# Performance work log

Hardware: AMD Instinct MI355X
Metric: run time of the kernel (lower is better)

## Reference

```python
import jax, jax.numpy as jnp
from jax import lax
import numpy as np


def _lstm_layer(x, Wih, Whh, bih, bhh):
    """Single-direction LSTM layer, PyTorch gate order (i, f, g, o).
    x: [B, T, D_in] -> hidden sequence [B, T, H]."""
    B, T, _ = x.shape
    H = Whh.shape[1]
    # Precompute input contribution for all timesteps: [B, T, 4H]
    xw = jnp.einsum('btd,gd->btg', x, Wih) + bih + bhh

    def step(carry, xt):
        h, c = carry
        gates = xt + h @ Whh.T  # [B, 4H]
        i, f, g, o = jnp.split(gates, 4, axis=-1)
        i = jax.nn.sigmoid(i)
        f = jax.nn.sigmoid(f)
        g = jnp.tanh(g)
        o = jax.nn.sigmoid(o)
        c = f * c + i * g
        h = o * jnp.tanh(c)
        return (h, c), h

    h0 = jnp.zeros((B, H), dtype=x.dtype)
    c0 = jnp.zeros((B, H), dtype=x.dtype)
    _, hs = lax.scan(step, (h0, c0), jnp.swapaxes(xw, 0, 1))  # [T, B, H]
    return jnp.swapaxes(hs, 0, 1)  # [B, T, H]


def setup_inputs() -> dict:
    key = jax.random.key(0)
    ks = jax.random.split(key, 9)
    B, T, D, H = 64, 2048, 256, 128
    s = 1.0 / np.sqrt(H)  # PyTorch uniform(-1/sqrt(H), 1/sqrt(H)) init scale
    u = lambda k, shp: jax.random.uniform(k, shp, jnp.float32, -s, s)
    return {
        'x': jax.random.normal(ks[0], (B, T, D), jnp.float32),
        'Wih0': u(ks[1], (4 * H, D)),
        'Whh0': u(ks[2], (4 * H, H)),
        'bih0': u(ks[3], (4 * H,)),
        'bhh0': u(ks[4], (4 * H,)),
        'Wih1': u(ks[5], (4 * H, H)),
        'Whh1': u(ks[6], (4 * H, H)),
        'bih1': u(ks[7], (4 * H,)),
        'bhh1': u(ks[8], (4 * H,)),
    }


def reference(x, Wih0, Whh0, bih0, bhh0, Wih1, Whh1, bih1, bhh1):
    # 2-layer stacked LSTM; inter-layer dropout (p=0.1) is identity at eval.
    h1 = _lstm_layer(x, Wih0, Whh0, bih0, bhh0)
    h2 = _lstm_layer(h1, Wih1, Whh1, bih1, bhh1)
    return h2
```

## Files before the change

kernel.cpp:

```cpp
#include <hip/hip_runtime.h>
#include <hip/hip_bf16.h>

#define H 128
#define FOURH 512
#define BATCH 64
#define SEQ 2048
#define TC SEQ

typedef _Float16 half8 __attribute__((ext_vector_type(8)));
typedef float f32x4 __attribute__((ext_vector_type(4)));

__global__ void prep_kernel(const float* __restrict__ Wih0,
                            const float* __restrict__ bih0, const float* __restrict__ bhh0,
                            const float* __restrict__ bih1, const float* __restrict__ bhh1,
                            float* __restrict__ Wt0,
                            float* __restrict__ b0, float* __restrict__ b1,
                            int* __restrict__ flags) {
    int id = blockIdx.x * 256 + threadIdx.x;
    const int N0 = 256 * 512;
    if (id < N0) {
        int k = id >> 9, n = id & 511;
        Wt0[id] = Wih0[n * 256 + k];
    } else if (id < N0 + 512) {
        int i = id - N0;
        b0[i] = bih0[i] + bhh0[i];
    } else if (id < N0 + 1024) {
        int i = id - (N0 + 512);
        b1[i] = bih1[i] + bhh1[i];
    } else if (id < N0 + 1024 + 8) {
        flags[id - (N0 + 1024)] = 0;
    }
}

#define BM 128
#define BN 128
#define BK 32

__global__ __launch_bounds__(256) void gemm_bias_kernel(
    const float* __restrict__ A, int lda, int rowsPerBatch, int t0,
    const float* __restrict__ Bt, const float* __restrict__ bias,
    float* __restrict__ G, int K, int tcShift)
{
    __shared__ float As[BK][BM + 4];
    __shared__ float Bs[BK][BN];

    const int tid = threadIdx.x;
    const int m0 = blockIdx.y * BM;
    const int n0 = blockIdx.x * BN;
    const int tm = tid >> 4;
    const int tn = tid & 15;
    const int tcMask = (1 << tcShift) - 1;

    const float* aptr[4];
    int ar[4], aq[4];
#pragma unroll
    for (int l = 0; l < 4; ++l) {
        int fidx = tid + l * 256;
        int r = fidx >> 3, q = fidx & 7;
        ar[l] = r; aq[l] = q;
        int m = m0 + r;
        int bi = m >> tcShift;
        int tl = m & tcMask;
        aptr[l] = A + ((size_t)bi * rowsPerBatch + t0 + tl) * lda + q * 4;
    }
    int bkk[4], bq[4];
#pragma unroll
    for (int l = 0; l < 4; ++l) {
        int fidx = tid + l * 256;
        bkk[l] = fidx >> 5; bq[l] = fidx & 31;
    }

    float acc[2][2][4][4];
#pragma unroll
    for (int ri = 0; ri < 2; ++ri)
#pragma unroll
        for (int ci = 0; ci < 2; ++ci)
#pragma unroll
            for (int i = 0; i < 4; ++i)
#pragma unroll
                for (int j = 0; j < 4; ++j) acc[ri][ci][i][j] = 0.f;

    for (int k0 = 0; k0 < K; k0 += BK) {
        __syncthreads();
#pragma unroll
        for (int l = 0; l < 4; ++l) {
            float4 v = *(const float4*)(aptr[l] + k0);
            As[aq[l] * 4 + 0][ar[l]] = v.x;
            As[aq[l] * 4 + 1][ar[l]] = v.y;
            As[aq[l] * 4 + 2][ar[l]] = v.z;
            As[aq[l] * 4 + 3][ar[l]] = v.w;
        }
#pragma unroll
        for (int l = 0; l < 4; ++l) {
            float4 v = *(const float4*)(Bt + (size_t)(k0 + bkk[l]) * FOURH + n0 + bq[l] * 4);
            *(float4*)&Bs[bkk[l]][bq[l] * 4] = v;
        }
        __syncthreads();
#pragma unroll
        for (int kk = 0; kk < BK; ++kk) {
            float a[8], bb[8];
            *(float4*)&a[0] = *(const float4*)&As[kk][tm * 4];
            *(float4*)&a[4] = *(const float4*)&As[kk][64 + tm * 4];
            *(float4*)&bb[0] = *(const float4*)&Bs[kk][tn * 4];
            *(float4*)&bb[4] = *(const float4*)&Bs[kk][64 + tn * 4];
#pragma unroll
            for (int ri = 0; ri < 2; ++ri)
#pragma unroll
                for (int i = 0; i < 4; ++i)
#pragma unroll
                    for (int ci = 0; ci < 2; ++ci)
#pragma unroll
                        for (int j = 0; j < 4; ++j)
                            acc[ri][ci][i][j] = fmaf(a[ri * 4 + i], bb[ci * 4 + j], acc[ri][ci][i][j]);
        }
    }

    float4 bv0 = *(const float4*)&bias[n0 + tn * 4];
    float4 bv1 = *(const float4*)&bias[n0 + 64 + tn * 4];
#pragma unroll
    for (int ri = 0; ri < 2; ++ri)
#pragma unroll
        for (int i = 0; i < 4; ++i) {
            int m = m0 + ri * 64 + tm * 4 + i;
            float* gp = G + (size_t)m * FOURH + n0;
            float4 o0 = make_float4(acc[ri][0][i][0] + bv0.x, acc[ri][0][i][1] + bv0.y,
                                    acc[ri][0][i][2] + bv0.z, acc[ri][0][i][3] + bv0.w);
            float4 o1 = make_float4(acc[ri][1][i][0] + bv1.x, acc[ri][1][i][1] + bv1.y,
                                    acc[ri][1][i][2] + bv1.z, acc[ri][1][i][3] + bv1.w);
            *(float4*)(gp + tn * 4) = o0;
            *(float4*)(gp + 64 + tn * 4) = o1;
        }
}

__device__ __forceinline__ float sigmoid_f(float x) {
    return __builtin_amdgcn_rcpf(1.f + __expf(-x));
}
__device__ __forceinline__ float tanh_f(float x) {
    return 1.f - 2.f * __builtin_amdgcn_rcpf(__expf(2.f * x) + 1.f);
}

#define LDS_BARRIER()                                                \
    do {                                                             \
        asm volatile("s_waitcnt lgkmcnt(0)" ::: "memory");           \
        __builtin_amdgcn_s_barrier();                                \
        __builtin_amdgcn_sched_barrier(0);                           \
    } while (0)

__global__ __launch_bounds__(512, 2) void lstm_fused_kernel(
    const float* __restrict__ G,
    const float* __restrict__ Whh0,
    const float* __restrict__ Wih1,
    const float* __restrict__ Whh1,
    const float* __restrict__ b1,
    _Float16* __restrict__ h1p,
    float* __restrict__ out,
    int* __restrict__ flags)
{
    const int tid = threadIdx.x;
    const int w  = tid >> 6;
    const int l  = tid & 63;
    const int li = l & 15;
    const int q  = l >> 4;
    const int u  = 16 * w + li;
    const int b0 = q * 2;
    const int ab = ((li >> 2) * 2) + (li & 1);

    __shared__ _Float16 hbuf[2][8][136];
    __shared__ float houtb[8][8][132];

    if (blockIdx.x < 8) {
        const int g = blockIdx.x;

        half8 Bf[4][4];
#pragma unroll
        for (int tl = 0; tl < 4; ++tl)
#pragma unroll
            for (int kf = 0; kf < 4; ++kf) {
                const float* wp = Whh0 + (size_t)(tl * 128 + u) * H + kf * 32 + q * 8;
                float4 v0 = *(const float4*)wp;
                float4 v1 = *(const float4*)(wp + 4);
                half8 b;
                b[0] = (_Float16)v0.x; b[1] = (_Float16)v0.y;
                b[2] = (_Float16)v0.z; b[3] = (_Float16)v0.w;
                b[4] = (_Float16)v1.x; b[5] = (_Float16)v1.y;
                b[6] = (_Float16)v1.z; b[7] = (_Float16)v1.w;
                Bf[tl][kf] = b;
            }

        float c0 = 0.f, c1 = 0.f, h0 = 0.f, h1v = 0.f;
        hbuf[0][b0][u]     = (_Float16)0.f;
        hbuf[0][b0 + 1][u] = (_Float16)0.f;

        const float* gb = G + (size_t)(8 * g) * TC * FOURH;
        const int voff0 = b0 * TC * FOURH + u;
        const int voff1 = (b0 + 1) * TC * FOURH + u;

        float G0[8], G1[8], G2[8], G3[8];
        const float* gld = gb;
#pragma unroll
        for (int tl = 0; tl < 4; ++tl) {
            G0[tl * 2 + 0] = gld[voff0 + tl * H];
            G0[tl * 2 + 1] = gld[voff1 + tl * H];
        }
        gld += FOURH;
#pragma unroll
        for (int tl = 0; tl < 4; ++tl) {
            G1[tl * 2 + 0] = gld[voff0 + tl * H];
            G1[tl * 2 + 1] = gld[voff1 + tl * H];
        }
        gld += FOURH;
#pragma unroll
        for (int tl = 0; tl < 4; ++tl) {
            G2[tl * 2 + 0] = gld[voff0 + tl * H];
            G2[tl * 2 + 1] = gld[voff1 + tl * H];
        }
        gld += FOURH;
#pragma unroll
        for (int tl = 0; tl < 4; ++tl) {
            G3[tl * 2 + 0] = gld[voff0 + tl * H];
            G3[tl * 2 + 1] = gld[voff1 + tl * H];
        }
        gld += FOURH;

        _Float16* php = h1p + (size_t)(8 * g + b0) * H + u;
        __syncthreads();

#define P_STEP(PB, GR)                                                            \
    {                                                                             \
        half8 Afr[4];                                                             \
        _Pragma("unroll")                                                         \
        for (int kf = 0; kf < 4; ++kf)                                            \
            Afr[kf] = *(const half8*)&hbuf[PB][ab][kf * 32 + q * 8];              \
        f32x4 acc[4];                                                             \
        _Pragma("unroll")                                                         \
        for (int tl = 0; tl < 4; ++tl) {                                          \
            acc[tl][0] = GR[tl * 2 + 0]; acc[tl][1] = GR[tl * 2 + 1];             \
            acc[tl][2] = 0.f;            acc[tl][3] = 0.f;                        \
        }                                                                         \
        _Pragma("unroll")                                                         \
        for (int tl = 0; tl < 4; ++tl) {                                          \
            GR[tl * 2 + 0] = gld[voff0 + tl * H];                                 \
            GR[tl * 2 + 1] = gld[voff1 + tl * H];                                 \
        }                                                                         \
        gld += FOURH;                                                             \
        _Pragma("unroll")                                                         \
        for (int kf = 0; kf < 4; ++kf)                                            \
            _Pragma("unroll")                                                     \
            for (int tl = 0; tl < 4; ++tl)                                        \
                acc[tl] = __builtin_amdgcn_mfma_f32_16x16x32_f16(Afr[kf], Bf[tl][kf], acc[tl], 0, 0, 0); \
        {                                                                         \
            float ig = sigmoid_f(acc[0][0]);                                      \
            float fg = sigmoid_f(acc[1][0]);                                      \
            float gg = tanh_f(acc[2][0]);                                         \
            float og = sigmoid_f(acc[3][0]);                                      \
            c0 = fmaf(fg, c0, ig * gg);                                           \
            h0 = og * tanh_f(c0);                                                 \
            float ig1 = sigmoid_f(acc[0][1]);                                     \
            float fg1 = sigmoid_f(acc[1][1]);                                     \
            float gg1 = tanh_f(acc[2][1]);                                        \
            float og1 = sigmoid_f(acc[3][1]);                                     \
            c1 = fmaf(fg1, c1, ig1 * gg1);                                        \
            h1v = og1 * tanh_f(c1);                                               \
        }                                                                         \
        hbuf[PB ^ 1][b0][u]     = (_Float16)h0;                                   \
        hbuf[PB ^ 1][b0 + 1][u] = (_Float16)h1v;                                  \
        php[0]   = (_Float16)h0;                                                  \
        php[128] = (_Float16)h1v;                                                 \
        php += BATCH * H;                                                         \
        LDS_BARRIER();                                                            \
    }

        for (int s4 = 0; s4 < TC; s4 += 4) {
            P_STEP(0, G0)
            P_STEP(1, G1)
            P_STEP(0, G2)
            P_STEP(1, G3)
            if ((s4 & 15) == 12) {
                __threadfence();
                __syncthreads();
                if (tid == 0)
                    __hip_atomic_store(&flags[g], s4 + 4, __ATOMIC_RELEASE,
                                       __HIP_MEMORY_SCOPE_AGENT);
            }
        }
#undef P_STEP
    } else {
        const int g = blockIdx.x - 8;

        half8 Bf[4][8];
#pragma unroll
        for (int tl = 0; tl < 4; ++tl)
#pragma unroll
            for (int kf = 0; kf < 8; ++kf) {
                const float* base = (kf < 4) ? Wih1 : Whh1;
                int kk = (kf & 3) * 32 + q * 8;
                const float* wp = base + (size_t)(tl * 128 + u) * H + kk;
                float4 v0 = *(const float4*)wp;
                float4 v1 = *(const float4*)(wp + 4);
                half8 b;
                b[0] = (_Float16)v0.x; b[1] = (_Float16)v0.y;
                b[2] = (_Float16)v0.z; b[3] = (_Float16)v0.w;
                b[4] = (_Float16)v1.x; b[5] = (_Float16)v1.y;
                b[6] = (_Float16)v1.z; b[7] = (_Float16)v1.w;
                Bf[tl][kf] = b;
            }

        float bv[4];
#pragma unroll
        for (int tl = 0; tl < 4; ++tl) bv[tl] = b1[tl * 128 + u];

        float c0 = 0.f, c1 = 0.f, h0, h1v;
        hbuf[0][b0][u]     = (_Float16)0.f;
        hbuf[0][b0 + 1][u] = (_Float16)0.f;

        const _Float16* h1pG = h1p + (size_t)(8 * g + ab) * H + q * 8;
        float* houtBase = out + (size_t)(8 * g) * SEQ * H;

        if (tid == 0) {
            while (__hip_atomic_load(&flags[g], __ATOMIC_ACQUIRE,
                                     __HIP_MEMORY_SCOPE_AGENT) < 32)
                __builtin_amdgcn_s_sleep(2);
        }
        __syncthreads();

        half8 Af0[4], Af1[4];
#pragma unroll
        for (int kf = 0; kf < 4; ++kf)
            Af0[kf] = *(const half8*)(h1pG + kf * 32);
        {
            const _Float16* hp = h1pG + (size_t)(BATCH * H);
#pragma unroll
            for (int kf = 0; kf < 4; ++kf)
                Af1[kf] = *(const half8*)(hp + kf * 32);
        }

#define C_STEP(S, PB, AfU)                                                        \
    {                                                                             \
        half8 Ah[4];                                                              \
        _Pragma("unroll")                                                         \
        for (int kf = 0; kf < 4; ++kf)                                            \
            Ah[kf] = *(const half8*)&hbuf[PB][ab][kf * 32 + q * 8];               \
        f32x4 acc[4];                                                             \
        _Pragma("unroll")                                                         \
        for (int tl = 0; tl < 4; ++tl) {                                          \
            acc[tl][0] = bv[tl]; acc[tl][1] = bv[tl];                             \
            acc[tl][2] = bv[tl]; acc[tl][3] = bv[tl];                             \
        }                                                                         \
        _Pragma("unroll")                                                         \
        for (int kf = 0; kf < 4; ++kf)                                            \
            _Pragma("unroll")                                                     \
            for (int tl = 0; tl < 4; ++tl)                                        \
                acc[tl] = __builtin_amdgcn_mfma_f32_16x16x32_f16(AfU[kf], Bf[tl][kf], acc[tl], 0, 0, 0); \
        {                                                                         \
            int sn = (S) + 2; if (sn > TC - 1) sn = TC - 1;                       \
            const _Float16* hp = h1pG + (size_t)sn * (BATCH * H);                 \
            _Pragma("unroll")                                                     \
            for (int kf = 0; kf < 4; ++kf)                                        \
                AfU[kf] = *(const half8*)(hp + kf * 32);                          \
        }                                                                         \
        _Pragma("unroll")                                                         \
        for (int kf = 0; kf < 4; ++kf)                                            \
            _Pragma("unroll")                                                     \
            for (int tl = 0; tl < 4; ++tl)                                        \
                acc[tl] = __builtin_amdgcn_mfma_f32_16x16x32_f16(Ah[kf], Bf[tl][kf + 4], acc[tl], 0, 0, 0); \
        {                                                                         \
            float ig = sigmoid_f(acc[0][0]);                                      \
            float fg = sigmoid_f(acc[1][0]);                                      \
            float gg = tanh_f(acc[2][0]);                                         \
            float og = sigmoid_f(acc[3][0]);                                      \
            c0 = fmaf(fg, c0, ig * gg);                                           \
            h0 = og * tanh_f(c0);                                                 \
            float ig1 = sigmoid_f(acc[0][1]);                                     \
            float fg1 = sigmoid_f(acc[1][1]);                                     \
            float gg1 = tanh_f(acc[2][1]);                                        \
            float og1 = sigmoid_f(acc[3][1]);                                     \
            c1 = fmaf(fg1, c1, ig1 * gg1);                                        \
            h1v = og1 * tanh_f(c1);                                               \
        }                                                                         \
        hbuf[PB ^ 1][b0][u]     = (_Float16)h0;                                   \
        hbuf[PB ^ 1][b0 + 1][u] = (_Float16)h1v;                                  \
        houtb[(S) & 7][b0][u]     = h0;                                           \
        houtb[(S) & 7][b0 + 1][u] = h1v;                                          \
        LDS_BARRIER();                                                            \
    }

        for (int s4 = 0; s4 < TC; s4 += 4) {
            if (s4 && (s4 & 15) == 0) {
                if (tid == 0) {
                    int tgt = (s4 + 32 > TC) ? TC : s4 + 32;
                    while (__hip_atomic_load(&flags[g], __ATOMIC_ACQUIRE,
                                             __HIP_MEMORY_SCOPE_AGENT) < tgt)
                        __builtin_amdgcn_s_sleep(2);
                }
                __syncthreads();
            }
            C_STEP(s4 + 0, 0, Af0)
            C_STEP(s4 + 1, 1, Af1)
            C_STEP(s4 + 2, 0, Af0)
            C_STEP(s4 + 3, 1, Af1)
            if ((s4 & 7) == 4) {
                int sbase = s4 - 4;
#pragma unroll
                for (int k = 0; k < 4; ++k) {
                    int idx = k * 512 + tid;
                    int u4 = idx & 31;
                    int si = (idx >> 5) & 7;
                    int bi = idx >> 8;
                    float4 v = *(const float4*)&houtb[si][bi][u4 * 4];
                    float* dst = houtBase + (size_t)bi * SEQ * H
                               + (size_t)(sbase + si) * H + u4 * 4;
                    *(float4*)dst = v;
                }
                LDS_BARRIER();
            }
        }
#undef C_STEP
    }
}

extern "C" void kernel_launch(void* const* d_in, const int* in_sizes, int n_in,
                              void* d_out, int out_size, void* d_ws, size_t ws_size,
                              hipStream_t stream) {
    const float* x    = (const float*)d_in[0];
    const float* Wih0 = (const float*)d_in[1];
    const float* Whh0 = (const float*)d_in[2];
    const float* bih0 = (const float*)d_in[3];
    const float* bhh0 = (const float*)d_in[4];
    const float* Wih1 = (const float*)d_in[5];
    const float* Whh1 = (const float*)d_in[6];
    const float* bih1 = (const float*)d_in[7];
    const float* bhh1 = (const float*)d_in[8];
    float* out = (float*)d_out;

    char* ws = (char*)d_ws;
    size_t off = 0;
    auto carve = [&](size_t bytes) -> char* {
        char* p = ws + off;
        off += (bytes + 255) & ~(size_t)255;
        return p;
    };

    float*     Wt0   = (float*)carve(256 * 512 * 4);
    float*     b0v   = (float*)carve(512 * 4);
    float*     b1v   = (float*)carve(512 * 4);
    _Float16*  h1p   = (_Float16*)carve((size_t)SEQ * BATCH * H * 2);
    int*       flags = (int*)carve(8 * 4);
    float*     gbuf  = (float*)carve((size_t)BATCH * SEQ * FOURH * 4 + 16384);

    prep_kernel<<<517, 256, 0, stream>>>(Wih0, bih0, bhh0, bih1, bhh1, Wt0, b0v, b1v, flags);

    dim3 ggrid(FOURH / BN, (BATCH * SEQ) / BM);
    gemm_bias_kernel<<<ggrid, 256, 0, stream>>>(x, 256, SEQ, 0, Wt0, b0v, gbuf, 256, 11);

    lstm_fused_kernel<<<16, 512, 0, stream>>>(gbuf, Whh0, Wih1, Whh1, b1v,
                                              h1p, out, flags);
}
```

Measured before the change: 2.139 ms.

## Offload layer-1 input projection to dedicated blocks with ring-buffered pipeline

```diff
diff --git a/kernel.cpp b/kernel.cpp
--- a/kernel.cpp
+++ b/kernel.cpp
@@ -6,6 +6,9 @@
 #define BATCH 64
 #define SEQ 2048
 #define TC SEQ
+#define RH 1024
+#define RG 128
+#define CCH 32
 
 typedef _Float16 half8 __attribute__((ext_vector_type(8)));
 typedef float f32x4 __attribute__((ext_vector_type(4)));
@@ -27,7 +30,7 @@
     } else if (id < N0 + 1024) {
         int i = id - (N0 + 512);
         b1[i] = bih1[i] + bhh1[i];
-    } else if (id < N0 + 1024 + 8) {
+    } else if (id < N0 + 1024 + 24) {
         flags[id - (N0 + 1024)] = 0;
     }
 }
@@ -153,6 +156,7 @@
     const float* __restrict__ Whh1,
     const float* __restrict__ b1,
     _Float16* __restrict__ h1p,
+    float* __restrict__ G1r,
     float* __restrict__ out,
     int* __restrict__ flags)
 {
@@ -164,6 +168,10 @@
     const int u  = 16 * w + li;
     const int b0 = q * 2;
     const int ab = ((li >> 2) * 2) + (li & 1);
+
+    int* prodF = flags;
+    int* cF    = flags + 8;
+    int* consF = flags + 16;
 
     __shared__ _Float16 hbuf[2][8][136];
     __shared__ float houtb[8][8][132];
@@ -271,6 +279,18 @@
     }
 
         for (int s4 = 0; s4 < TC; s4 += 4) {
+            if ((s4 & 15) == 0 && s4) {
+                php = h1p + (size_t)(s4 & (RH - 1)) * (BATCH * H)
+                    + (size_t)(8 * g + b0) * H + u;
+                if (s4 >= RH) {
+                    if (tid == 0) {
+                        while (__hip_atomic_load(&cF[g], __ATOMIC_ACQUIRE,
+                                                 __HIP_MEMORY_SCOPE_AGENT) < s4 - (RH - CCH))
+                            __builtin_amdgcn_s_sleep(2);
+                    }
+                    __syncthreads();
+                }
+            }
             P_STEP(0, G0)
             P_STEP(1, G1)
             P_STEP(0, G2)
@@ -279,22 +299,20 @@
                 __threadfence();
                 __syncthreads();
                 if (tid == 0)
-                    __hip_atomic_store(&flags[g], s4 + 4, __ATOMIC_RELEASE,
+                    __hip_atomic_store(&prodF[g], s4 + 4, __ATOMIC_RELEASE,
                                        __HIP_MEMORY_SCOPE_AGENT);
             }
         }
 #undef P_STEP
-    } else {
+    } else if (blockIdx.x < 16) {
         const int g = blockIdx.x - 8;
 
-        half8 Bf[4][8];
+        half8 Bf[4][4];
 #pragma unroll
         for (int tl = 0; tl < 4; ++tl)
 #pragma unroll
-            for (int kf = 0; kf < 8; ++kf) {
-                const float* base = (kf < 4) ? Wih1 : Whh1;
-                int kk = (kf & 3) * 32 + q * 8;
-                const float* wp = base + (size_t)(tl * 128 + u) * H + kk;
+            for (int kf = 0; kf < 4; ++kf) {
+                const float* wp = Whh1 + (size_t)(tl * 128 + u) * H + kf * 32 + q * 8;
                 float4 v0 = *(const float4*)wp;
                 float4 v1 = *(const float4*)(wp + 4);
                 half8 b;
@@ -305,64 +323,59 @@
                 Bf[tl][kf] = b;
             }
 
-        float bv[4];
-#pragma unroll
-        for (int tl = 0; tl < 4; ++tl) bv[tl] = b1[tl * 128 + u];
-
         float c0 = 0.f, c1 = 0.f, h0, h1v;
         hbuf[0][b0][u]     = (_Float16)0.f;
         hbuf[0][b0 + 1][u] = (_Float16)0.f;
 
-        const _Float16* h1pG = h1p + (size_t)(8 * g + ab) * H + q * 8;
+        const int goff0 = (8 * g + b0) * FOURH + u;
+        const int goff1 = goff0 + FOURH;
         float* houtBase = out + (size_t)(8 * g) * SEQ * H;
 
         if (tid == 0) {
-            while (__hip_atomic_load(&flags[g], __ATOMIC_ACQUIRE,
+            while (__hip_atomic_load(&cF[g], __ATOMIC_ACQUIRE,
                                      __HIP_MEMORY_SCOPE_AGENT) < 32)
                 __builtin_amdgcn_s_sleep(2);
         }
         __syncthreads();
 
-        half8 Af0[4], Af1[4];
-#pragma unroll
-        for (int kf = 0; kf < 4; ++kf)
-            Af0[kf] = *(const half8*)(h1pG + kf * 32);
-        {
-            const _Float16* hp = h1pG + (size_t)(BATCH * H);
-#pragma unroll
-            for (int kf = 0; kf < 4; ++kf)
-                Af1[kf] = *(const half8*)(hp + kf * 32);
-        }
-
-#define C_STEP(S, PB, AfU)                                                        \
+        float G0[8], G1[8], G2[8], G3[8];
+#pragma unroll
+        for (int tl = 0; tl < 4; ++tl) {
+            G0[tl * 2 + 0] = G1r[(size_t)0 * (BATCH * FOURH) + goff0 + tl * H];
+            G0[tl * 2 + 1] = G1r[(size_t)0 * (BATCH * FOURH) + goff1 + tl * H];
+            G1[tl * 2 + 0] = G1r[(size_t)1 * (BATCH * FOURH) + goff0 + tl * H];
+            G1[tl * 2 + 1] = G1r[(size_t)1 * (BATCH * FOURH) + goff1 + tl * H];
+            G2[tl * 2 + 0] = G1r[(size_t)2 * (BATCH * FOURH) + goff0 + tl * H];
+            G2[tl * 2 + 1] = G1r[(size_t)2 * (BATCH * FOURH) + goff1 + tl * H];
+            G3[tl * 2 + 0] = G1r[(size_t)3 * (BATCH * FOURH) + goff0 + tl * H];
+            G3[tl * 2 + 1] = G1r[(size_t)3 * (BATCH * FOURH) + goff1 + tl * H];
+        }
+
+#define C_STEP(S, PB, GR)                                                         \
     {                                                                             \
-        half8 Ah[4];                                                              \
+        half8 Afr[4];                                                             \
         _Pragma("unroll")                                                         \
         for (int kf = 0; kf < 4; ++kf)                                            \
-            Ah[kf] = *(const half8*)&hbuf[PB][ab][kf * 32 + q * 8];               \
+            Afr[kf] = *(const half8*)&hbuf[PB][ab][kf * 32 + q * 8];              \
         f32x4 acc[4];                                                             \
         _Pragma("unroll")                                                         \
         for (int tl = 0; tl < 4; ++tl) {                                          \
-            acc[tl][0] = bv[tl]; acc[tl][1] = bv[tl];                             \
-            acc[tl][2] = bv[tl]; acc[tl][3] = bv[tl];                             \
+            acc[tl][0] = GR[tl * 2 + 0]; acc[tl][1] = GR[tl * 2 + 1];             \
+            acc[tl][2] = 0.f;            acc[tl][3] = 0.f;                        \
+        }                                                                         \
+        {                                                                         \
+            const float* gp = G1r + (size_t)(((S) + 4) & (RG - 1)) * (BATCH * FOURH); \
+            _Pragma("unroll")                                                     \
+            for (int tl = 0; tl < 4; ++tl) {                                      \
+                GR[tl * 2 + 0] = gp[goff0 + tl * H];                              \
+                GR[tl * 2 + 1] = gp[goff1 + tl * H];                              \
+            }                                                                     \
         }                                                                         \
         _Pragma("unroll")                                                         \
         for (int kf = 0; kf < 4; ++kf)                                            \
             _Pragma("unroll")                                                     \
             for (int tl = 0; tl < 4; ++tl)                                        \
-                acc[tl] = __builtin_amdgcn_mfma_f32_16x16x32_f16(AfU[kf], Bf[tl][kf], acc[tl], 0, 0, 0); \
-        {                                                                         \
-            int sn = (S) + 2; if (sn > TC - 1) sn = TC - 1;                       \
-            const _Float16* hp = h1pG + (size_t)sn * (BATCH * H);                 \
-            _Pragma("unroll")                                                     \
-            for (int kf = 0; kf < 4; ++kf)                                        \
-                AfU[kf] = *(const half8*)(hp + kf * 32);                          \
-        }                                                                         \
-        _Pragma("unroll")                                                         \
-        for (int kf = 0; kf < 4; ++kf)                                            \
-            _Pragma("unroll")                                                     \
-            for (int tl = 0; tl < 4; ++tl)                                        \
-                acc[tl] = __builtin_amdgcn_mfma_f32_16x16x32_f16(Ah[kf], Bf[tl][kf + 4], acc[tl], 0, 0, 0); \
+                acc[tl] = __builtin_amdgcn_mfma_f32_16x16x32_f16(Afr[kf], Bf[tl][kf], acc[tl], 0, 0, 0); \
         {                                                                         \
             float ig = sigmoid_f(acc[0][0]);                                      \
             float fg = sigmoid_f(acc[1][0]);                                      \
@@ -385,19 +398,20 @@
     }
 
         for (int s4 = 0; s4 < TC; s4 += 4) {
-            if (s4 && (s4 & 15) == 0) {
+            if ((s4 & 15) == 0 && s4) {
                 if (tid == 0) {
-                    int tgt = (s4 + 32 > TC) ? TC : s4 + 32;
-                    while (__hip_atomic_load(&flags[g], __ATOMIC_ACQUIRE,
+                    int tgt = (s4 + 20 + 31) & ~31;
+                    if (tgt > TC) tgt = TC;
+                    while (__hip_atomic_load(&cF[g], __ATOMIC_ACQUIRE,
                                              __HIP_MEMORY_SCOPE_AGENT) < tgt)
                         __builtin_amdgcn_s_sleep(2);
                 }
                 __syncthreads();
             }
-            C_STEP(s4 + 0, 0, Af0)
-            C_STEP(s4 + 1, 1, Af1)
-            C_STEP(s4 + 2, 0, Af0)
-            C_STEP(s4 + 3, 1, Af1)
+            C_STEP(s4 + 0, 0, G0)
+            C_STEP(s4 + 1, 1, G1)
+            C_STEP(s4 + 2, 0, G2)
+            C_STEP(s4 + 3, 1, G3)
             if ((s4 & 7) == 4) {
                 int sbase = s4 - 4;
 #pragma unroll
@@ -413,8 +427,88 @@
                 }
                 LDS_BARRIER();
             }
+            if ((s4 & 15) == 12) {
+                if (tid == 0)
+                    __hip_atomic_store(&consF[g], s4 + 4, __ATOMIC_RELEASE,
+                                       __HIP_MEMORY_SCOPE_AGENT);
+            }
         }
 #undef C_STEP
+    } else {
+        const int g = blockIdx.x - 16;
+
+        half8 Bf[4][4];
+#pragma unroll
+        for (int tl = 0; tl < 4; ++tl)
+#pragma unroll
+            for (int kf = 0; kf < 4; ++kf) {
+                const float* wp = Wih1 + (size_t)(tl * 128 + u) * H + kf * 32 + q * 8;
+                float4 v0 = *(const float4*)wp;
+                float4 v1 = *(const float4*)(wp + 4);
+                half8 b;
+                b[0] = (_Float16)v0.x; b[1] = (_Float16)v0.y;
+                b[2] = (_Float16)v0.z; b[3] = (_Float16)v0.w;
+                b[4] = (_Float16)v1.x; b[5] = (_Float16)v1.y;
+                b[6] = (_Float16)v1.z; b[7] = (_Float16)v1.w;
+                Bf[tl][kf] = b;
+            }
+
+        float bv[4];
+#pragma unroll
+        for (int tl = 0; tl < 4; ++tl) bv[tl] = b1[tl * 128 + u];
+
+        const int liB = li & 7;
+        const int dtl = li >> 3;
+        const int qd  = q >> 1;
+        const int qb  = (q & 1) * 4;
+
+        for (int c = 0; c < TC; c += CCH) {
+            if (tid == 0) {
+                while (__hip_atomic_load(&prodF[g], __ATOMIC_ACQUIRE,
+                                         __HIP_MEMORY_SCOPE_AGENT) < c + CCH)
+                    __builtin_amdgcn_s_sleep(2);
+                if (c >= RG) {
+                    while (__hip_atomic_load(&consF[g], __ATOMIC_ACQUIRE,
+                                             __HIP_MEMORY_SCOPE_AGENT) < c + CCH - RG)
+                        __builtin_amdgcn_s_sleep(2);
+                }
+            }
+            __syncthreads();
+#pragma unroll 2
+            for (int rt = 0; rt < 16; ++rt) {
+                const _Float16* ap = h1p
+                    + ((size_t)(((c + 2 * rt) & (RH - 1)) + dtl)) * (BATCH * H)
+                    + (size_t)(8 * g + liB) * H + q * 8;
+                half8 Af[4];
+#pragma unroll
+                for (int kf = 0; kf < 4; ++kf)
+                    Af[kf] = *(const half8*)(ap + kf * 32);
+                f32x4 acc[4];
+#pragma unroll
+                for (int tl = 0; tl < 4; ++tl) {
+                    acc[tl][0] = bv[tl]; acc[tl][1] = bv[tl];
+                    acc[tl][2] = bv[tl]; acc[tl][3] = bv[tl];
+                }
+#pragma unroll
+                for (int kf = 0; kf < 4; ++kf)
+#pragma unroll
+                    for (int tl = 0; tl < 4; ++tl)
+                        acc[tl] = __builtin_amdgcn_mfma_f32_16x16x32_f16(Af[kf], Bf[tl][kf], acc[tl], 0, 0, 0);
+                float* op = G1r
+                    + ((size_t)((c + 2 * rt) & (RG - 1)) + qd) * (BATCH * FOURH)
+                    + (size_t)(8 * g + qb) * FOURH + u;
+#pragma unroll
+                for (int tl = 0; tl < 4; ++tl)
+#pragma unroll
+                    for (int i = 0; i < 4; ++i)
+                        op[(size_t)i * FOURH + tl * H] = acc[tl][i];
+            }
+            __threadfence();
+            __syncthreads();
+            if (tid == 0)
+                __hip_atomic_store(&cF[g], c + CCH, __ATOMIC_RELEASE,
+                                   __HIP_MEMORY_SCOPE_AGENT);
+        }
     }
 }
 
@@ -443,8 +537,9 @@
     float*     Wt0   = (float*)carve(256 * 512 * 4);
     float*     b0v   = (float*)carve(512 * 4);
     float*     b1v   = (float*)carve(512 * 4);
-    _Float16*  h1p   = (_Float16*)carve((size_t)SEQ * BATCH * H * 2);
-    int*       flags = (int*)carve(8 * 4);
+    _Float16*  h1p   = (_Float16*)carve((size_t)RH * BATCH * H * 2);
+    int*       flags = (int*)carve(24 * 4);
+    float*     g1r   = (float*)carve((size_t)RG * BATCH * FOURH * 4);
     float*     gbuf  = (float*)carve((size_t)BATCH * SEQ * FOURH * 4 + 16384);
 
     prep_kernel<<<517, 256, 0, stream>>>(Wih0, bih0, bhh0, bih1, bhh1, Wt0, b0v, b1v, flags);
@@ -452,6 +547,6 @@
     dim3 ggrid(FOURH / BN, (BATCH * SEQ) / BM);
     gemm_bias_kernel<<<ggrid, 256, 0, stream>>>(x, 256, SEQ, 0, Wt0, b0v, gbuf, 256, 11);
 
-    lstm_fused_kernel<<<16, 512, 0, stream>>>(gbuf, Whh0, Wih1, Whh1, b1v,
-                                              h1p, out, flags);
+    lstm_fused_kernel<<<24, 512, 0, stream>>>(gbuf, Whh0, Wih1, Whh1, b1v,
+                                              h1p, g1r, out, flags);
 }
```

New measurement: 2.517 ms. 1.18x slower.

## Fuse input-projection GEMM into LSTM kernel with chunked producer flags

Applied to the files above, without the earlier changes.

```diff
diff --git a/kernel.cpp b/kernel.cpp
--- a/kernel.cpp
+++ b/kernel.cpp
@@ -6,6 +6,8 @@
 #define BATCH 64
 #define SEQ 2048
 #define TC SEQ
+#define NCHUNK 128
+#define NGEMMB 224
 
 typedef _Float16 half8 __attribute__((ext_vector_type(8)));
 typedef float f32x4 __attribute__((ext_vector_type(4)));
@@ -27,109 +29,9 @@
     } else if (id < N0 + 1024) {
         int i = id - (N0 + 512);
         b1[i] = bih1[i] + bhh1[i];
-    } else if (id < N0 + 1024 + 8) {
+    } else if (id < N0 + 1024 + 8 + NCHUNK) {
         flags[id - (N0 + 1024)] = 0;
     }
-}
-
-#define BM 128
-#define BN 128
-#define BK 32
-
-__global__ __launch_bounds__(256) void gemm_bias_kernel(
-    const float* __restrict__ A, int lda, int rowsPerBatch, int t0,
-    const float* __restrict__ Bt, const float* __restrict__ bias,
-    float* __restrict__ G, int K, int tcShift)
-{
-    __shared__ float As[BK][BM + 4];
-    __shared__ float Bs[BK][BN];
-
-    const int tid = threadIdx.x;
-    const int m0 = blockIdx.y * BM;
-    const int n0 = blockIdx.x * BN;
-    const int tm = tid >> 4;
-    const int tn = tid & 15;
-    const int tcMask = (1 << tcShift) - 1;
-
-    const float* aptr[4];
-    int ar[4], aq[4];
-#pragma unroll
-    for (int l = 0; l < 4; ++l) {
-        int fidx = tid + l * 256;
-        int r = fidx >> 3, q = fidx & 7;
-        ar[l] = r; aq[l] = q;
-        int m = m0 + r;
-        int bi = m >> tcShift;
-        int tl = m & tcMask;
-        aptr[l] = A + ((size_t)bi * rowsPerBatch + t0 + tl) * lda + q * 4;
-    }
-    int bkk[4], bq[4];
-#pragma unroll
-    for (int l = 0; l < 4; ++l) {
-        int fidx = tid + l * 256;
-        bkk[l] = fidx >> 5; bq[l] = fidx & 31;
-    }
-
-    float acc[2][2][4][4];
-#pragma unroll
-    for (int ri = 0; ri < 2; ++ri)
-#pragma unroll
-        for (int ci = 0; ci < 2; ++ci)
-#pragma unroll
-            for (int i = 0; i < 4; ++i)
-#pragma unroll
-                for (int j = 0; j < 4; ++j) acc[ri][ci][i][j] = 0.f;
-
-    for (int k0 = 0; k0 < K; k0 += BK) {
-        __syncthreads();
-#pragma unroll
-        for (int l = 0; l < 4; ++l) {
-            float4 v = *(const float4*)(aptr[l] + k0);
-            As[aq[l] * 4 + 0][ar[l]] = v.x;
-            As[aq[l] * 4 + 1][ar[l]] = v.y;
-            As[aq[l] * 4 + 2][ar[l]] = v.z;
-            As[aq[l] * 4 + 3][ar[l]] = v.w;
-        }
-#pragma unroll
-        for (int l = 0; l < 4; ++l) {
-            float4 v = *(const float4*)(Bt + (size_t)(k0 + bkk[l]) * FOURH + n0 + bq[l] * 4);
-            *(float4*)&Bs[bkk[l]][bq[l] * 4] = v;
-        }
-        __syncthreads();
-#pragma unroll
-        for (int kk = 0; kk < BK; ++kk) {
-            float a[8], bb[8];
-            *(float4*)&a[0] = *(const float4*)&As[kk][tm * 4];
-            *(float4*)&a[4] = *(const float4*)&As[kk][64 + tm * 4];
-            *(float4*)&bb[0] = *(const float4*)&Bs[kk][tn * 4];
-            *(float4*)&bb[4] = *(const float4*)&Bs[kk][64 + tn * 4];
-#pragma unroll
-            for (int ri = 0; ri < 2; ++ri)
-#pragma unroll
-                for (int i = 0; i < 4; ++i)
-#pragma unroll
-                    for (int ci = 0; ci < 2; ++ci)
-#pragma unroll
-                        for (int j = 0; j < 4; ++j)
-                            acc[ri][ci][i][j] = fmaf(a[ri * 4 + i], bb[ci * 4 + j], acc[ri][ci][i][j]);
-        }
-    }
-
-    float4 bv0 = *(const float4*)&bias[n0 + tn * 4];
-    float4 bv1 = *(const float4*)&bias[n0 + 64 + tn * 4];
-#pragma unroll
-    for (int ri = 0; ri < 2; ++ri)
-#pragma unroll
-        for (int i = 0; i < 4; ++i) {
-            int m = m0 + ri * 64 + tm * 4 + i;
-            float* gp = G + (size_t)m * FOURH + n0;
-            float4 o0 = make_float4(acc[ri][0][i][0] + bv0.x, acc[ri][0][i][1] + bv0.y,
-                                    acc[ri][0][i][2] + bv0.z, acc[ri][0][i][3] + bv0.w);
-            float4 o1 = make_float4(acc[ri][1][i][0] + bv1.x, acc[ri][1][i][1] + bv1.y,
-                                    acc[ri][1][i][2] + bv1.z, acc[ri][1][i][3] + bv1.w);
-            *(float4*)(gp + tn * 4) = o0;
-            *(float4*)(gp + 64 + tn * 4) = o1;
-        }
 }
 
 __device__ __forceinline__ float sigmoid_f(float x) {
@@ -146,8 +48,15 @@
         __builtin_amdgcn_sched_barrier(0);                           \
     } while (0)
 
+#define BM 128
+#define BN 128
+#define BK 32
+
 __global__ __launch_bounds__(512, 2) void lstm_fused_kernel(
-    const float* __restrict__ G,
+    const float* __restrict__ x,
+    const float* __restrict__ Wt0,
+    const float* __restrict__ b0sum,
+    float* __restrict__ G,
     const float* __restrict__ Whh0,
     const float* __restrict__ Wih1,
     const float* __restrict__ Whh1,
@@ -157,6 +66,103 @@
     int* __restrict__ flags)
 {
     const int tid = threadIdx.x;
+
+    int* prodF     = flags;
+    int* chunkDone = flags + 8;
+
+    __shared__ _Float16 hbuf[2][8][136];
+    __shared__ float As[BK][BM + 4];
+    __shared__ float Bs[BK][BN];
+
+    if (blockIdx.x >= 16) {
+        const int j   = blockIdx.x - 16;
+        const int sub = j & 31;
+        const int cls = j >> 5;
+        const int by  = sub >> 2;
+        const int bx  = sub & 3;
+        const int n0  = bx * BN;
+        const int tm  = tid >> 5;
+        const int tn  = tid & 31;
+
+        int ar[2], aq[2], bkk[2], bq[2];
+#pragma unroll
+        for (int l = 0; l < 2; ++l) {
+            int fidx = tid + l * 512;
+            ar[l] = fidx >> 3; aq[l] = fidx & 7;
+            bkk[l] = fidx >> 5; bq[l] = fidx & 31;
+        }
+        float4 bv = *(const float4*)&b0sum[n0 + tn * 4];
+
+        for (int c = cls; c < NCHUNK; c += 7) {
+            const float* aptr[2];
+#pragma unroll
+            for (int l = 0; l < 2; ++l) {
+                int rl = by * BM + ar[l];
+                int b = rl >> 4;
+                int t = c * 16 + (rl & 15);
+                aptr[l] = x + ((size_t)b * SEQ + t) * 256 + aq[l] * 4;
+            }
+            float acc[2][4][4];
+#pragma unroll
+            for (int rh = 0; rh < 2; ++rh)
+#pragma unroll
+                for (int i = 0; i < 4; ++i)
+#pragma unroll
+                    for (int jj = 0; jj < 4; ++jj) acc[rh][i][jj] = 0.f;
+
+            for (int k0 = 0; k0 < 256; k0 += BK) {
+                __syncthreads();
+#pragma unroll
+                for (int l = 0; l < 2; ++l) {
+                    float4 v = *(const float4*)(aptr[l] + k0);
+                    As[aq[l] * 4 + 0][ar[l]] = v.x;
+                    As[aq[l] * 4 + 1][ar[l]] = v.y;
+                    As[aq[l] * 4 + 2][ar[l]] = v.z;
+                    As[aq[l] * 4 + 3][ar[l]] = v.w;
+                }
+#pragma unroll
+                for (int l = 0; l < 2; ++l) {
+                    float4 v = *(const float4*)(Wt0 + (size_t)(k0 + bkk[l]) * FOURH + n0 + bq[l] * 4);
+                    *(float4*)&Bs[bkk[l]][bq[l] * 4] = v;
+                }
+                __syncthreads();
+#pragma unroll
+                for (int kk = 0; kk < BK; ++kk) {
+                    float a[8], bb[4];
+                    *(float4*)&a[0] = *(const float4*)&As[kk][tm * 4];
+                    *(float4*)&a[4] = *(const float4*)&As[kk][64 + tm * 4];
+                    *(float4*)&bb[0] = *(const float4*)&Bs[kk][tn * 4];
+#pragma unroll
+                    for (int rh = 0; rh < 2; ++rh)
+#pragma unroll
+                        for (int i = 0; i < 4; ++i)
+#pragma unroll
+                            for (int jj = 0; jj < 4; ++jj)
+                                acc[rh][i][jj] = fmaf(a[rh * 4 + i], bb[jj], acc[rh][i][jj]);
+                }
+            }
+#pragma unroll
+            for (int rh = 0; rh < 2; ++rh)
+#pragma unroll
+                for (int i = 0; i < 4; ++i) {
+                    int rl = by * BM + rh * 64 + tm * 4 + i;
+                    int b = rl >> 4;
+                    int t = c * 16 + (rl & 15);
+                    float* gp = G + ((size_t)b * SEQ + t) * FOURH + n0 + tn * 4;
+                    float4 o = make_float4(acc[rh][i][0] + bv.x, acc[rh][i][1] + bv.y,
+                                           acc[rh][i][2] + bv.z, acc[rh][i][3] + bv.w);
+                    *(float4*)gp = o;
+                }
+            __syncthreads();
+            if (tid == 0) {
+                __threadfence();
+                __hip_atomic_fetch_add(&chunkDone[c], 1, __ATOMIC_RELEASE,
+                                       __HIP_MEMORY_SCOPE_AGENT);
+            }
+        }
+        return;
+    }
+
     const int w  = tid >> 6;
     const int l  = tid & 63;
     const int li = l & 15;
@@ -165,8 +171,17 @@
     const int b0 = q * 2;
     const int ab = ((li >> 2) * 2) + (li & 1);
 
-    __shared__ _Float16 hbuf[2][8][136];
-    __shared__ float houtb[8][8][132];
+#define WAIT_FLAG(ptr, tgtv)                                                   \
+    do {                                                                       \
+        if (tid == 0) {                                                        \
+            while (__hip_atomic_load((ptr), __ATOMIC_RELAXED,                  \
+                                     __HIP_MEMORY_SCOPE_AGENT) < (tgtv))       \
+                __builtin_amdgcn_s_sleep(4);                                   \
+            (void)__hip_atomic_load((ptr), __ATOMIC_ACQUIRE,                   \
+                                    __HIP_MEMORY_SCOPE_AGENT);                 \
+        }                                                                      \
+        __syncthreads();                                                       \
+    } while (0)
 
     if (blockIdx.x < 8) {
         const int g = blockIdx.x;
@@ -195,6 +210,8 @@
         const int voff0 = b0 * TC * FOURH + u;
         const int voff1 = (b0 + 1) * TC * FOURH + u;
 
+        WAIT_FLAG(&chunkDone[0], 32);
+
         float G0[8], G1[8], G2[8], G3[8];
         const float* gld = gb;
 #pragma unroll
@@ -223,7 +240,6 @@
         gld += FOURH;
 
         _Float16* php = h1p + (size_t)(8 * g + b0) * H + u;
-        __syncthreads();
 
 #define P_STEP(PB, GR)                                                            \
     {                                                                             \
@@ -271,15 +287,20 @@
     }
 
         for (int s4 = 0; s4 < TC; s4 += 4) {
+            if ((s4 & 15) == 0) {
+                int k = (s4 >> 4) + 1;
+                if (k > NCHUNK - 1) k = NCHUNK - 1;
+                WAIT_FLAG(&chunkDone[k], 32);
+            }
             P_STEP(0, G0)
             P_STEP(1, G1)
             P_STEP(0, G2)
             P_STEP(1, G3)
-            if ((s4 & 15) == 12) {
+            if ((s4 & 31) == 28) {
                 __threadfence();
                 __syncthreads();
                 if (tid == 0)
-                    __hip_atomic_store(&flags[g], s4 + 4, __ATOMIC_RELEASE,
+                    __hip_atomic_store(&prodF[g], s4 + 4, __ATOMIC_RELEASE,
                                        __HIP_MEMORY_SCOPE_AGENT);
             }
         }
@@ -314,14 +335,10 @@
         hbuf[0][b0 + 1][u] = (_Float16)0.f;
 
         const _Float16* h1pG = h1p + (size_t)(8 * g + ab) * H + q * 8;
-        float* houtBase = out + (size_t)(8 * g) * SEQ * H;
-
-        if (tid == 0) {
-            while (__hip_atomic_load(&flags[g], __ATOMIC_ACQUIRE,
-                                     __HIP_MEMORY_SCOPE_AGENT) < 32)
-                __builtin_amdgcn_s_sleep(2);
-        }
-        __syncthreads();
+        float* op0 = out + (size_t)(8 * g + b0) * SEQ * H + u;
+        float* op1 = out + (size_t)(8 * g + b0 + 1) * SEQ * H + u;
+
+        WAIT_FLAG(&prodF[g], 64);
 
         half8 Af0[4], Af1[4];
 #pragma unroll
@@ -379,43 +396,25 @@
         }                                                                         \
         hbuf[PB ^ 1][b0][u]     = (_Float16)h0;                                   \
         hbuf[PB ^ 1][b0 + 1][u] = (_Float16)h1v;                                  \
-        houtb[(S) & 7][b0][u]     = h0;                                           \
-        houtb[(S) & 7][b0 + 1][u] = h1v;                                          \
+        op0[0] = h0;                                                              \
+        op1[0] = h1v;                                                             \
+        op0 += H; op1 += H;                                                       \
         LDS_BARRIER();                                                            \
     }
 
         for (int s4 = 0; s4 < TC; s4 += 4) {
-            if (s4 && (s4 & 15) == 0) {
-                if (tid == 0) {
-                    int tgt = (s4 + 32 > TC) ? TC : s4 + 32;
-                    while (__hip_atomic_load(&flags[g], __ATOMIC_ACQUIRE,
-                                             __HIP_MEMORY_SCOPE_AGENT) < tgt)
-                        __builtin_amdgcn_s_sleep(2);
-                }
-                __syncthreads();
+            if (s4 && (s4 & 31) == 0) {
+                int tgt = s4 + 64; if (tgt > TC) tgt = TC;
+                WAIT_FLAG(&prodF[g], tgt);
             }
             C_STEP(s4 + 0, 0, Af0)
             C_STEP(s4 + 1, 1, Af1)
             C_STEP(s4 + 2, 0, Af0)
             C_STEP(s4 + 3, 1, Af1)
-            if ((s4 & 7) == 4) {
-                int sbase = s4 - 4;
-#pragma unroll
-                for (int k = 0; k < 4; ++k) {
-                    int idx = k * 512 + tid;
-                    int u4 = idx & 31;
-                    int si = (idx >> 5) & 7;
-                    int bi = idx >> 8;
-                    float4 v = *(const float4*)&houtb[si][bi][u4 * 4];
-                    float* dst = houtBase + (size_t)bi * SEQ * H
-                               + (size_t)(sbase + si) * H + u4 * 4;
-                    *(float4*)dst = v;
-                }
-                LDS_BARRIER();
-            }
         }
 #undef C_STEP
     }
+#undef WAIT_FLAG
 }
 
 extern "C" void kernel_launch(void* const* d_in, const int* in_sizes, int n_in,
@@ -444,14 +443,12 @@
     float*     b0v   = (float*)carve(512 * 4);
     float*     b1v   = (float*)carve(512 * 4);
     _Float16*  h1p   = (_Float16*)carve((size_t)SEQ * BATCH * H * 2);
-    int*       flags = (int*)carve(8 * 4);
+    int*       flags = (int*)carve((8 + NCHUNK) * 4);
     float*     gbuf  = (float*)carve((size_t)BATCH * SEQ * FOURH * 4 + 16384);
 
     prep_kernel<<<517, 256, 0, stream>>>(Wih0, bih0, bhh0, bih1, bhh1, Wt0, b0v, b1v, flags);
 
-    dim3 ggrid(FOURH / BN, (BATCH * SEQ) / BM);
-    gemm_bias_kernel<<<ggrid, 256, 0, stream>>>(x, 256, SEQ, 0, Wt0, b0v, gbuf, 256, 11);
-
-    lstm_fused_kernel<<<16, 512, 0, stream>>>(gbuf, Whh0, Wih1, Whh1, b1v,
-                                              h1p, out, flags);
+    lstm_fused_kernel<<<240, 512, 0, stream>>>(x, Wt0, b0v, gbuf,
+                                               Whh0, Wih1, Whh1, b1v,
+                                               h1p, out, flags);
 }
```

New measurement: 2.071 ms. -3.2%, faster.

## Replace scalar FP32 input GEMM with split-FP16 MFMA; store LSTM outputs directly

Applied to the files above, without the earlier changes.

```diff
diff --git a/kernel.cpp b/kernel.cpp
--- a/kernel.cpp
+++ b/kernel.cpp
@@ -13,123 +13,86 @@
 __global__ void prep_kernel(const float* __restrict__ Wih0,
                             const float* __restrict__ bih0, const float* __restrict__ bhh0,
                             const float* __restrict__ bih1, const float* __restrict__ bhh1,
-                            float* __restrict__ Wt0,
+                            _Float16* __restrict__ w0h, _Float16* __restrict__ w0l,
                             float* __restrict__ b0, float* __restrict__ b1,
                             int* __restrict__ flags) {
     int id = blockIdx.x * 256 + threadIdx.x;
-    const int N0 = 256 * 512;
-    if (id < N0) {
-        int k = id >> 9, n = id & 511;
-        Wt0[id] = Wih0[n * 256 + k];
-    } else if (id < N0 + 512) {
-        int i = id - N0;
+    const int NW = 512 * 256;
+    if (id < NW) {
+        float v = Wih0[id];
+        _Float16 hi = (_Float16)v;
+        w0h[id] = hi;
+        w0l[id] = (_Float16)(v - (float)hi);
+    } else if (id < NW + 512) {
+        int i = id - NW;
         b0[i] = bih0[i] + bhh0[i];
-    } else if (id < N0 + 1024) {
-        int i = id - (N0 + 512);
+    } else if (id < NW + 1024) {
+        int i = id - (NW + 512);
         b1[i] = bih1[i] + bhh1[i];
-    } else if (id < N0 + 1024 + 8) {
-        flags[id - (N0 + 1024)] = 0;
-    }
-}
-
-#define BM 128
-#define BN 128
-#define BK 32
-
-__global__ __launch_bounds__(256) void gemm_bias_kernel(
-    const float* __restrict__ A, int lda, int rowsPerBatch, int t0,
-    const float* __restrict__ Bt, const float* __restrict__ bias,
-    float* __restrict__ G, int K, int tcShift)
+    } else if (id < NW + 1024 + 8) {
+        flags[id - (NW + 1024)] = 0;
+    }
+}
+
+__global__ __launch_bounds__(512) void gemm0_mfma_kernel(
+    const float* __restrict__ x,
+    const _Float16* __restrict__ w0h,
+    const _Float16* __restrict__ w0l,
+    const float* __restrict__ b0sum,
+    float* __restrict__ G)
 {
-    __shared__ float As[BK][BM + 4];
-    __shared__ float Bs[BK][BN];
-
+    const int j   = blockIdx.x;
+    const int tc  = j >> 5;
+    const int sub = j & 31;
+    const int by  = sub >> 2;
+    const int bx  = sub & 3;
+    const int n0  = bx * 128;
     const int tid = threadIdx.x;
-    const int m0 = blockIdx.y * BM;
-    const int n0 = blockIdx.x * BN;
-    const int tm = tid >> 4;
-    const int tn = tid & 15;
-    const int tcMask = (1 << tcShift) - 1;
-
-    const float* aptr[4];
-    int ar[4], aq[4];
-#pragma unroll
-    for (int l = 0; l < 4; ++l) {
-        int fidx = tid + l * 256;
-        int r = fidx >> 3, q = fidx & 7;
-        ar[l] = r; aq[l] = q;
-        int m = m0 + r;
-        int bi = m >> tcShift;
-        int tl = m & tcMask;
-        aptr[l] = A + ((size_t)bi * rowsPerBatch + t0 + tl) * lda + q * 4;
-    }
-    int bkk[4], bq[4];
-#pragma unroll
-    for (int l = 0; l < 4; ++l) {
-        int fidx = tid + l * 256;
-        bkk[l] = fidx >> 5; bq[l] = fidx & 31;
-    }
-
-    float acc[2][2][4][4];
-#pragma unroll
-    for (int ri = 0; ri < 2; ++ri)
-#pragma unroll
-        for (int ci = 0; ci < 2; ++ci)
-#pragma unroll
-            for (int i = 0; i < 4; ++i)
-#pragma unroll
-                for (int j = 0; j < 4; ++j) acc[ri][ci][i][j] = 0.f;
-
-    for (int k0 = 0; k0 < K; k0 += BK) {
-        __syncthreads();
-#pragma unroll
-        for (int l = 0; l < 4; ++l) {
-            float4 v = *(const float4*)(aptr[l] + k0);
-            As[aq[l] * 4 + 0][ar[l]] = v.x;
-            As[aq[l] * 4 + 1][ar[l]] = v.y;
-            As[aq[l] * 4 + 2][ar[l]] = v.z;
-            As[aq[l] * 4 + 3][ar[l]] = v.w;
-        }
-#pragma unroll
-        for (int l = 0; l < 4; ++l) {
-            float4 v = *(const float4*)(Bt + (size_t)(k0 + bkk[l]) * FOURH + n0 + bq[l] * 4);
-            *(float4*)&Bs[bkk[l]][bq[l] * 4] = v;
-        }
-        __syncthreads();
-#pragma unroll
-        for (int kk = 0; kk < BK; ++kk) {
-            float a[8], bb[8];
-            *(float4*)&a[0] = *(const float4*)&As[kk][tm * 4];
-            *(float4*)&a[4] = *(const float4*)&As[kk][64 + tm * 4];
-            *(float4*)&bb[0] = *(const float4*)&Bs[kk][tn * 4];
-            *(float4*)&bb[4] = *(const float4*)&Bs[kk][64 + tn * 4];
-#pragma unroll
-            for (int ri = 0; ri < 2; ++ri)
-#pragma unroll
-                for (int i = 0; i < 4; ++i)
-#pragma unroll
-                    for (int ci = 0; ci < 2; ++ci)
-#pragma unroll
-                        for (int j = 0; j < 4; ++j)
-                            acc[ri][ci][i][j] = fmaf(a[ri * 4 + i], bb[ci * 4 + j], acc[ri][ci][i][j]);
-        }
-    }
-
-    float4 bv0 = *(const float4*)&bias[n0 + tn * 4];
-    float4 bv1 = *(const float4*)&bias[n0 + 64 + tn * 4];
-#pragma unroll
-    for (int ri = 0; ri < 2; ++ri)
-#pragma unroll
-        for (int i = 0; i < 4; ++i) {
-            int m = m0 + ri * 64 + tm * 4 + i;
-            float* gp = G + (size_t)m * FOURH + n0;
-            float4 o0 = make_float4(acc[ri][0][i][0] + bv0.x, acc[ri][0][i][1] + bv0.y,
-                                    acc[ri][0][i][2] + bv0.z, acc[ri][0][i][3] + bv0.w);
-            float4 o1 = make_float4(acc[ri][1][i][0] + bv1.x, acc[ri][1][i][1] + bv1.y,
-                                    acc[ri][1][i][2] + bv1.z, acc[ri][1][i][3] + bv1.w);
-            *(float4*)(gp + tn * 4) = o0;
-            *(float4*)(gp + 64 + tn * 4) = o1;
-        }
+    const int wv  = tid >> 6;
+    const int l   = tid & 63;
+    const int li  = l & 15;
+    const int q   = l >> 4;
+    const int b   = 8 * by + wv;
+    const int t0  = tc * 16;
+
+    f32x4 acc[8];
+#pragma unroll
+    for (int ct = 0; ct < 8; ++ct) {
+        float bv = b0sum[n0 + ct * 16 + li];
+        acc[ct][0] = bv; acc[ct][1] = bv; acc[ct][2] = bv; acc[ct][3] = bv;
+    }
+
+    const float* xp = x + ((size_t)b * SEQ + t0 + li) * 256 + q * 8;
+
+    for (int kf = 0; kf < 8; ++kf) {
+        float4 v0 = *(const float4*)(xp + kf * 32);
+        float4 v1 = *(const float4*)(xp + kf * 32 + 4);
+        half8 ah, al;
+        ah[0] = (_Float16)v0.x; al[0] = (_Float16)(v0.x - (float)ah[0]);
+        ah[1] = (_Float16)v0.y; al[1] = (_Float16)(v0.y - (float)ah[1]);
+        ah[2] = (_Float16)v0.z; al[2] = (_Float16)(v0.z - (float)ah[2]);
+        ah[3] = (_Float16)v0.w; al[3] = (_Float16)(v0.w - (float)ah[3]);
+        ah[4] = (_Float16)v1.x; al[4] = (_Float16)(v1.x - (float)ah[4]);
+        ah[5] = (_Float16)v1.y; al[5] = (_Float16)(v1.y - (float)ah[5]);
+        ah[6] = (_Float16)v1.z; al[6] = (_Float16)(v1.z - (float)ah[6]);
+        ah[7] = (_Float16)v1.w; al[7] = (_Float16)(v1.w - (float)ah[7]);
+#pragma unroll
+        for (int ct = 0; ct < 8; ++ct) {
+            size_t woff = (size_t)(n0 + ct * 16 + li) * 256 + kf * 32 + q * 8;
+            half8 bh = *(const half8*)(w0h + woff);
+            half8 bl = *(const half8*)(w0l + woff);
+            acc[ct] = __builtin_amdgcn_mfma_f32_16x16x32_f16(al, bh, acc[ct], 0, 0, 0);
+            acc[ct] = __builtin_amdgcn_mfma_f32_16x16x32_f16(ah, bl, acc[ct], 0, 0, 0);
+            acc[ct] = __builtin_amdgcn_mfma_f32_16x16x32_f16(ah, bh, acc[ct], 0, 0, 0);
+        }
+    }
+
+    float* gp = G + ((size_t)b * SEQ + t0 + q * 4) * FOURH + n0 + li;
+#pragma unroll
+    for (int ct = 0; ct < 8; ++ct)
+#pragma unroll
+        for (int i = 0; i < 4; ++i)
+            gp[(size_t)i * FOURH + ct * 16] = acc[ct][i];
 }
 
 __device__ __forceinline__ float sigmoid_f(float x) {
@@ -166,7 +129,6 @@
     const int ab = ((li >> 2) * 2) + (li & 1);
 
     __shared__ _Float16 hbuf[2][8][136];
-    __shared__ float houtb[8][8][132];
 
     if (blockIdx.x < 8) {
         const int g = blockIdx.x;
@@ -314,7 +276,8 @@
         hbuf[0][b0 + 1][u] = (_Float16)0.f;
 
         const _Float16* h1pG = h1p + (size_t)(8 * g + ab) * H + q * 8;
-        float* houtBase = out + (size_t)(8 * g) * SEQ * H;
+        float* op0 = out + (size_t)(8 * g + b0) * SEQ * H + u;
+        float* op1 = out + (size_t)(8 * g + b0 + 1) * SEQ * H + u;
 
         if (tid == 0) {
             while (__hip_atomic_load(&flags[g], __ATOMIC_ACQUIRE,
@@ -379,13 +342,14 @@
         }                                                                         \
         hbuf[PB ^ 1][b0][u]     = (_Float16)h0;                                   \
         hbuf[PB ^ 1][b0 + 1][u] = (_Float16)h1v;                                  \
-        houtb[(S) & 7][b0][u]     = h0;                                           \
-        houtb[(S) & 7][b0 + 1][u] = h1v;                                          \
+        op0[0] = h0;                                                              \
+        op1[0] = h1v;                                                             \
+        op0 += H; op1 += H;                                                       \
         LDS_BARRIER();                                                            \
     }
 
         for (int s4 = 0; s4 < TC; s4 += 4) {
-            if (s4 && (s4 & 15) == 0) {
+            if (s4 && (s4 & 31) == 0) {
                 if (tid == 0) {
                     int tgt = (s4 + 32 > TC) ? TC : s4 + 32;
                     while (__hip_atomic_load(&flags[g], __ATOMIC_ACQUIRE,
@@ -398,21 +362,6 @@
             C_STEP(s4 + 1, 1, Af1)
             C_STEP(s4 + 2, 0, Af0)
             C_STEP(s4 + 3, 1, Af1)
-            if ((s4 & 7) == 4) {
-                int sbase = s4 - 4;
-#pragma unroll
-                for (int k = 0; k < 4; ++k) {
-                    int idx = k * 512 + tid;
-                    int u4 = idx & 31;
-                    int si = (idx >> 5) & 7;
-                    int bi = idx >> 8;
-                    float4 v = *(const float4*)&houtb[si][bi][u4 * 4];
-                    float* dst = houtBase + (size_t)bi * SEQ * H
-                               + (size_t)(sbase + si) * H + u4 * 4;
-                    *(float4*)dst = v;
-                }
-                LDS_BARRIER();
-            }
         }
 #undef C_STEP
     }
@@ -440,17 +389,18 @@
         return p;
     };
 
-    float*     Wt0   = (float*)carve(256 * 512 * 4);
+    _Float16*  w0h   = (_Float16*)carve(512 * 256 * 2);
+    _Float16*  w0l   = (_Float16*)carve(512 * 256 * 2);
     float*     b0v   = (float*)carve(512 * 4);
     float*     b1v   = (float*)carve(512 * 4);
     _Float16*  h1p   = (_Float16*)carve((size_t)SEQ * BATCH * H * 2);
     int*       flags = (int*)carve(8 * 4);
     float*     gbuf  = (float*)carve((size_t)BATCH * SEQ * FOURH * 4 + 16384);
 
-    prep_kernel<<<517, 256, 0, stream>>>(Wih0, bih0, bhh0, bih1, bhh1, Wt0, b0v, b1v, flags);
-
-    dim3 ggrid(FOURH / BN, (BATCH * SEQ) / BM);
-    gemm_bias_kernel<<<ggrid, 256, 0, stream>>>(x, 256, SEQ, 0, Wt0, b0v, gbuf, 256, 11);
+    prep_kernel<<<517, 256, 0, stream>>>(Wih0, bih0, bhh0, bih1, bhh1,
+                                         w0h, w0l, b0v, b1v, flags);
+
+    gemm0_mfma_kernel<<<4096, 512, 0, stream>>>(x, w0h, w0l, b0v, gbuf);
 
     lstm_fused_kernel<<<16, 512, 0, stream>>>(gbuf, Whh0, Wih1, Whh1, b1v,
                                               h1p, out, flags);
```

Result: slower. 2.344 ms (+9.6%).
